# Kernel tuning notes

Hardware: AMD Instinct MI355X
Metric: run time of the kernel (lower is better)

## Reference

```python
import jax, jax.numpy as jnp
import numpy as np

B, N, L, G, H, D, DIM = 32, 512, 4096, 128, 8, 1, 64
ALPHA = 3.0


def setup_inputs() -> dict:
    key = jax.random.key(0)
    k = jax.random.split(key, 8)
    return {
        "idx": jnp.arange(N, dtype=jnp.int32),
        "queries": jnp.zeros((1,), jnp.float32),
        "keys": jnp.zeros((1,), jnp.float32),
        "values": jnp.zeros((1,), jnp.float32),
        "attn_mask": jnp.zeros((1,), jnp.bool_),
        "x": jax.random.normal(k[0], (B, N, L), jnp.float32),
        "emb1": jax.random.normal(k[1], (N, DIM), jnp.float32),
        "emb2": jax.random.normal(k[2], (N, DIM), jnp.float32),
        "lin1_w": jax.random.normal(k[3], (DIM, DIM), jnp.float32) / np.sqrt(DIM).astype(np.float32),
        "lin1_b": jnp.zeros((DIM,), jnp.float32),
        "lin2_w": jax.random.normal(k[4], (DIM, DIM), jnp.float32) / np.sqrt(DIM).astype(np.float32),
        "lin2_b": jnp.zeros((DIM,), jnp.float32),
        "mlp_w": jax.random.normal(k[5], (L, H * D), jnp.float32) / np.sqrt(L).astype(np.float32),
        "mlp_b": jnp.zeros((H * D,), jnp.float32),
        "W_sel": jax.random.normal(k[6], (H, G, D), jnp.float32),
    }


def reference(idx, queries, keys, values, attn_mask, x,
              emb1, emb2, lin1_w, lin1_b, lin2_w, lin2_b,
              mlp_w, mlp_b, W_sel):
    # --- graph_constructor.forward(idx) ---
    n1 = jnp.tanh(ALPHA * (emb1[idx] @ lin1_w + lin1_b))   # [N, DIM]
    n2 = jnp.tanh(ALPHA * (emb2[idx] @ lin2_w + lin2_b))   # [N, DIM]
    a = n1 @ n2.T - n2 @ n1.T                               # [N, N]
    adj = jnp.tanh(ALPHA * a)
    # topk (k == nsensor in GlobalAttention) + scatter mask; noise in the
    # original only perturbs tie-breaking of indices, values are set to 1.
    kk = idx.shape[0]
    _, top_idx = jax.lax.top_k(adj, kk)
    rows = jnp.arange(adj.shape[0])[:, None]
    mask = jnp.zeros_like(adj).at[rows, top_idx].set(1.0)
    adj = adj * mask

    # --- SelectAttention(x) ---
    b, n, l = x.shape
    newx = jnp.tanh(x.reshape(b * n, l) @ mlp_w + mlp_b)    # [(B N), H*D]
    # faithful raw row-major reshape (matches torch.reshape semantics)
    newx = newx.reshape(b, H, n, D)                          # [B, H, N, D]
    sel = jax.nn.relu(jnp.einsum('bhnd,hgd->bhng', newx, W_sel))[:, 0]  # [B, N, G]

    # --- combine ---
    scores = jnp.einsum('ls,blg->bsg', adj, sel)             # [B, N, G]
    series = jax.nn.softmax(scores, axis=-1)
    V = jnp.einsum('bls,blg->bsg', x, series)                # [B, L, G]
    return V
```

## Files before the change

### kernel.cpp

```cpp
#include <hip/hip_runtime.h>
#include <hip/hip_bf16.h>
#include <math.h>

#define BB 32
#define NN 512
#define LL 4096
#define GG 128
#define DD 64
#define AS 36
#define RS2 36

typedef __attribute__((ext_vector_type(4))) float f32x4;
typedef __attribute__((ext_vector_type(8))) short bf16x8;
typedef __attribute__((ext_vector_type(4))) unsigned u32x4;
typedef __attribute__((ext_vector_type(4))) unsigned short u16x4;

__device__ inline float sx(float v, int m) { return __shfl_xor(v, m, 64); }

__global__ __launch_bounds__(64) void ga_nodes(
    const int* __restrict__ idx,
    const float* __restrict__ emb1, const float* __restrict__ emb2,
    const float* __restrict__ w1, const float* __restrict__ b1,
    const float* __restrict__ w2, const float* __restrict__ b2,
    float* __restrict__ n1, float* __restrict__ n2,
    float* __restrict__ n1T, float* __restrict__ n2T) {
  int i = blockIdx.x;
  int d = threadIdx.x;
  int ii = idx[i];
  const float* e1 = emb1 + ii * DD;
  const float* e2 = emb2 + ii * DD;
  float a1 = 0.f, a2 = 0.f;
  #pragma unroll 8
  for (int k = 0; k < DD; ++k) {
    a1 += e1[k] * w1[k * DD + d];
    a2 += e2[k] * w2[k * DD + d];
  }
  float v1 = tanhf(3.f * (a1 + b1[d]));
  float v2 = tanhf(3.f * (a2 + b2[d]));
  n1[i * DD + d] = v1;
  n2[i * DD + d] = v2;
  n1T[(size_t)d * NN + i] = v1;
  n2T[(size_t)d * NN + i] = v2;
}

__global__ __launch_bounds__(256) void ga_adjT(
    const float* __restrict__ n1, const float* __restrict__ n2,
    const float* __restrict__ n1T, const float* __restrict__ n2T,
    __hip_bfloat16* __restrict__ adjT16) {
  int l0 = blockIdx.x * 64, s0 = blockIdx.y * 16;
  int tid = threadIdx.x;
  int ll = tid & 63;
  int sw = __builtin_amdgcn_readfirstlane(tid >> 6);
  int l = l0 + ll;

  float d1[4] = {0.f, 0.f, 0.f, 0.f}, d2[4] = {0.f, 0.f, 0.f, 0.f};
  #pragma unroll
  for (int kb = 0; kb < 4; ++kb) {
    float a1[16], a2[16];
    #pragma unroll
    for (int k = 0; k < 16; ++k) {
      a1[k] = n1T[(size_t)(kb * 16 + k) * NN + l];
      a2[k] = n2T[(size_t)(kb * 16 + k) * NN + l];
    }
    #pragma unroll
    for (int si = 0; si < 4; ++si) {
      int s = s0 + sw * 4 + si;
      const float* s1 = n1 + (size_t)s * DD + kb * 16;
      const float* s2 = n2 + (size_t)s * DD + kb * 16;
      #pragma unroll
      for (int k = 0; k < 16; ++k) {
        d1[si] += a1[k] * s2[k];
        d2[si] += a2[k] * s1[k];
      }
    }
  }
  #pragma unroll
  for (int si = 0; si < 4; ++si) {
    int s = s0 + sw * 4 + si;
    adjT16[(size_t)s * NN + l] =
        __float2bfloat16(tanhf(3.f * (d1[si] - d2[si])));
  }
}

__global__ __launch_bounds__(256) void ga_mlp(
    const float* __restrict__ x, const float* __restrict__ mlp_w,
    const float* __restrict__ mlp_b, const float* __restrict__ wsel,
    __hip_bfloat16* __restrict__ RT) {
  int b = blockIdx.y;
  int j0 = blockIdx.x * 4;
  int n0 = j0 * 8;
  int tid = threadIdx.x;
  const float* xb = x + (size_t)b * NN * LL;

  float acc[4][8];
  #pragma unroll
  for (int r = 0; r < 4; ++r)
    #pragma unroll
    for (int c = 0; c < 8; ++c) acc[r][c] = 0.f;

  #pragma unroll 4
  for (int it = 0; it < 16; ++it) {
    int l = it * 256 + tid;
    float4 w0 = *(const float4*)(mlp_w + (size_t)l * 8);
    float4 w1 = *(const float4*)(mlp_w + (size_t)l * 8 + 4);
    float wv[8] = {w0.x, w0.y, w0.z, w0.w, w1.x, w1.y, w1.z, w1.w};
    float xv[4];
    #pragma unroll
    for (int r = 0; r < 4; ++r) xv[r] = xb[(size_t)(j0 + r) * LL + l];
    #pragma unroll
    for (int r = 0; r < 4; ++r)
      #pragma unroll
      for (int c = 0; c < 8; ++c) acc[r][c] += xv[r] * wv[c];
  }
  #pragma unroll
  for (int r = 0; r < 4; ++r)
    #pragma unroll
    for (int c = 0; c < 8; ++c) {
      float v = acc[r][c];
      for (int off = 32; off; off >>= 1) v += __shfl_down(v, off);
      acc[r][c] = v;
    }
  __shared__ float red[4][32];
  __shared__ float tl[32];
  int lane = tid & 63, wave = tid >> 6;
  if (lane == 0) {
    #pragma unroll
    for (int r = 0; r < 4; ++r)
      #pragma unroll
      for (int c = 0; c < 8; ++c) red[wave][r * 8 + c] = acc[r][c];
  }
  __syncthreads();
  if (tid < 32) {
    float s = red[0][tid] + red[1][tid] + red[2][tid] + red[3][tid];
    tl[tid] = tanhf(s + mlp_b[tid & 7]);
  }
  __syncthreads();
  unsigned short* rp = (unsigned short*)RT + (size_t)b * GG * NN + n0;
  #pragma unroll
  for (int itw = 0; itw < 4; ++itw) {
    int f = itw * 256 + tid;
    int g = f >> 3, c4 = (f & 7) * 4;
    float w = wsel[g];
    u16x4 pk;
    #pragma unroll
    for (int k = 0; k < 4; ++k)
      pk[k] = __bfloat16_as_ushort(__float2bfloat16(fmaxf(tl[c4 + k] * w, 0.f)));
    *(u16x4*)(rp + (size_t)g * NN + c4) = pk;
  }
}

__global__ __launch_bounds__(256) void ga_scores_mfma(
    const __hip_bfloat16* __restrict__ adjT16,
    const __hip_bfloat16* __restrict__ RT,
    __hip_bfloat16* __restrict__ seriesT) {
  int b = blockIdx.y;
  int s0 = blockIdx.x * 64;
  int tid = threadIdx.x;
  __shared__ unsigned As[64 * AS];
  __shared__ unsigned Bs[128 * AS];
  int wave = tid >> 6, lane = tid & 63, q = lane >> 4, mrow = lane & 15;
  const unsigned short* ap = (const unsigned short*)adjT16;
  const unsigned short* bp = (const unsigned short*)RT + (size_t)b * GG * NN;

  f32x4 acc[8];
  #pragma unroll
  for (int nf = 0; nf < 8; ++nf) acc[nf] = (f32x4){0.f, 0.f, 0.f, 0.f};

  for (int l0 = 0; l0 < NN; l0 += 64) {
    #pragma unroll
    for (int it = 0; it < 2; ++it) {
      int ci = it * 256 + tid;
      int row = ci >> 3, part = ci & 7;
      *(u32x4*)&As[row * AS + part * 4] =
          *(const u32x4*)(ap + (size_t)(s0 + row) * NN + l0 + part * 8);
    }
    #pragma unroll
    for (int it = 0; it < 4; ++it) {
      int ci = it * 256 + tid;
      int row = ci >> 3, part = ci & 7;
      *(u32x4*)&Bs[row * AS + part * 4] =
          *(const u32x4*)(bp + (size_t)row * NN + l0 + part * 8);
    }
    __syncthreads();
    #pragma unroll
    for (int ks = 0; ks < 2; ++ks) {
      bf16x8 af = *(const bf16x8*)&As[(wave * 16 + mrow) * AS + ks * 16 + q * 4];
      #pragma unroll
      for (int nf = 0; nf < 8; ++nf) {
        bf16x8 bfr = *(const bf16x8*)&Bs[(nf * 16 + mrow) * AS + ks * 16 + q * 4];
        acc[nf] = __builtin_amdgcn_mfma_f32_16x16x32_bf16(af, bfr, acc[nf], 0, 0, 0);
      }
    }
    __syncthreads();
  }

  unsigned short* sT = (unsigned short*)seriesT + (size_t)b * GG * NN;
  f32x4 mx = acc[0];
  #pragma unroll
  for (int nf = 1; nf < 8; ++nf)
    #pragma unroll
    for (int r = 0; r < 4; ++r) mx[r] = fmaxf(mx[r], acc[nf][r]);
  #pragma unroll
  for (int m = 1; m <= 8; m <<= 1)
    #pragma unroll
    for (int r = 0; r < 4; ++r) mx[r] = fmaxf(mx[r], sx(mx[r], m));
  f32x4 sum = (f32x4){0.f, 0.f, 0.f, 0.f};
  #pragma unroll
  for (int nf = 0; nf < 8; ++nf)
    #pragma unroll
    for (int r = 0; r < 4; ++r) {
      float e = __expf(acc[nf][r] - mx[r]);
      acc[nf][r] = e;
      sum[r] += e;
    }
  #pragma unroll
  for (int m = 1; m <= 8; m <<= 1)
    #pragma unroll
    for (int r = 0; r < 4; ++r) sum[r] += sx(sum[r], m);
  f32x4 inv;
  #pragma unroll
  for (int r = 0; r < 4; ++r) inv[r] = 1.f / sum[r];
  int sbase = s0 + wave * 16 + q * 4;
  #pragma unroll
  for (int nf = 0; nf < 8; ++nf) {
    u16x4 pk;
    #pragma unroll
    for (int r = 0; r < 4; ++r)
      pk[r] = __bfloat16_as_ushort(__float2bfloat16(acc[nf][r] * inv[r]));
    *(u16x4*)(sT + (size_t)(nf * 16 + mrow) * NN + sbase) = pk;
  }
}

__global__ __launch_bounds__(256) void ga_V_mfma(
    const float* __restrict__ x, const __hip_bfloat16* __restrict__ seriesT,
    float* __restrict__ out) {
  int b = blockIdx.y;
  int p0 = blockIdx.x * 128;
  int tid = threadIdx.x;
  __shared__ unsigned St[128 * RS2];
  int wave = tid >> 6, lane = tid & 63, q = lane >> 4, mrow = lane & 15;
  int sgrow = tid >> 1;
  int sc0 = (tid & 1) * 4;
  const float* xb = x + (size_t)b * NN * LL;
  const unsigned short* sb = (const unsigned short*)seriesT + (size_t)b * GG * NN;
  int pcol = p0 + wave * 32 + mrow;

  f32x4 acc[2][8];
  #pragma unroll
  for (int mf = 0; mf < 2; ++mf)
    #pragma unroll
    for (int nf = 0; nf < 8; ++nf) acc[mf][nf] = (f32x4){0.f, 0.f, 0.f, 0.f};

  #pragma unroll 1
  for (int l0 = 0; l0 < NN; l0 += 64) {
    float xv[2][2][8];
    #pragma unroll
    for (int mf = 0; mf < 2; ++mf)
      #pragma unroll
      for (int ks = 0; ks < 2; ++ks) {
        const float* xp = xb + (size_t)(l0 + ks * 32 + q * 8) * LL + pcol + mf * 16;
        #pragma unroll
        for (int jj = 0; jj < 8; ++jj) xv[mf][ks][jj] = xp[(size_t)jj * LL];
      }
    u32x4 sv[4];
    #pragma unroll
    for (int k = 0; k < 4; ++k)
      sv[k] = *(const u32x4*)(sb + (size_t)sgrow * NN + l0 + (sc0 + k) * 8);
    #pragma unroll
    for (int k = 0; k < 4; ++k)
      *(u32x4*)&St[sgrow * RS2 + (sc0 + k) * 4] = sv[k];
    __syncthreads();

    bf16x8 af[2][2];
    #pragma unroll
    for (int mf = 0; mf < 2; ++mf)
      #pragma unroll
      for (int ks = 0; ks < 2; ++ks) {
        unsigned w[4];
        #pragma unroll
        for (int t = 0; t < 4; ++t) {
          __hip_bfloat162 pk = __float22bfloat162_rn(
              make_float2(xv[mf][ks][2 * t], xv[mf][ks][2 * t + 1]));
          w[t] = *(unsigned*)&pk;
        }
        af[mf][ks] = *(bf16x8*)w;
      }
    #pragma unroll
    for (int ks = 0; ks < 2; ++ks)
      #pragma unroll
      for (int nf = 0; nf < 8; ++nf) {
        bf16x8 bfr = *(const bf16x8*)&St[(nf * 16 + mrow) * RS2 + ks * 16 + q * 4];
        acc[0][nf] = __builtin_amdgcn_mfma_f32_16x16x32_bf16(af[0][ks], bfr, acc[0][nf], 0, 0, 0);
        acc[1][nf] = __builtin_amdgcn_mfma_f32_16x16x32_bf16(af[1][ks], bfr, acc[1][nf], 0, 0, 0);
      }
    __syncthreads();
  }

  #pragma unroll
  for (int mf = 0; mf < 2; ++mf) {
    int pb = p0 + wave * 32 + mf * 16 + q * 4;
    #pragma unroll
    for (int nf = 0; nf < 8; ++nf) {
      int g = nf * 16 + mrow;
      float* op = out + ((size_t)b * LL + pb) * GG + g;
      #pragma unroll
      for (int r = 0; r < 4; ++r) op[(size_t)r * GG] = acc[mf][nf][r];
    }
  }
}

extern "C" void kernel_launch(void* const* d_in, const int* in_sizes, int n_in,
                              void* d_out, int out_size, void* d_ws, size_t ws_size,
                              hipStream_t stream) {
  const int*   idx    = (const int*)d_in[0];
  const float* x      = (const float*)d_in[5];
  const float* emb1   = (const float*)d_in[6];
  const float* emb2   = (const float*)d_in[7];
  const float* lin1_w = (const float*)d_in[8];
  const float* lin1_b = (const float*)d_in[9];
  const float* lin2_w = (const float*)d_in[10];
  const float* lin2_b = (const float*)d_in[11];
  const float* mlp_w  = (const float*)d_in[12];
  const float* mlp_b  = (const float*)d_in[13];
  const float* W_sel  = (const float*)d_in[14];
  float* out = (float*)d_out;

  float* ws = (float*)d_ws;
  float* n1  = ws;
  float* n2  = ws + 32768;
  float* n1T = ws + 65536;
  float* n2T = ws + 98304;
  __hip_bfloat16* adjT16  = (__hip_bfloat16*)(ws + 131072);
  __hip_bfloat16* RT      = (__hip_bfloat16*)(ws + 262144);
  __hip_bfloat16* seriesT = (__hip_bfloat16*)(ws + 1310720);

  ga_nodes<<<NN, 64, 0, stream>>>(idx, emb1, emb2, lin1_w, lin1_b,
                                  lin2_w, lin2_b, n1, n2, n1T, n2T);
  ga_adjT<<<dim3(NN / 64, NN / 16), 256, 0, stream>>>(n1, n2, n1T, n2T, adjT16);
  ga_mlp<<<dim3(16, BB), 256, 0, stream>>>(x, mlp_w, mlp_b, W_sel, RT);
  ga_scores_mfma<<<dim3(8, BB), 256, 0, stream>>>(adjT16, RT, seriesT);
  ga_V_mfma<<<dim3(LL / 128, BB), 256, 0, stream>>>(x, seriesT, out);
}
```

Baseline: 114.7 us.

## Fuse node embedding into adjacency kernel and build sel operand on the fly

Merges the node-embedding kernel into the adjacency kernel. Each block recomputes the 80 node rows it needs into shared memory, which removes one launch and the n1/n2 transposed buffers. The MLP kernel now writes only the 32 tanh values per row, and the scores MFMA kernel builds the relu(t*W_sel) bf16 B-fragments in registers instead of reading a materialized RT tensor from global memory. This cuts global traffic and a launch, but adds redundant embedding compute across blocks and extra ALU work inside the MFMA loop.

```diff
diff --git a/kernel.cpp b/kernel.cpp
--- a/kernel.cpp
+++ b/kernel.cpp
@@ -17,75 +17,74 @@
 
 __device__ inline float sx(float v, int m) { return __shfl_xor(v, m, 64); }
 
-__global__ __launch_bounds__(64) void ga_nodes(
+__global__ __launch_bounds__(256) void ga_graph(
     const int* __restrict__ idx,
     const float* __restrict__ emb1, const float* __restrict__ emb2,
     const float* __restrict__ w1, const float* __restrict__ b1,
     const float* __restrict__ w2, const float* __restrict__ b2,
-    float* __restrict__ n1, float* __restrict__ n2,
-    float* __restrict__ n1T, float* __restrict__ n2T) {
-  int i = blockIdx.x;
-  int d = threadIdx.x;
-  int ii = idx[i];
-  const float* e1 = emb1 + ii * DD;
-  const float* e2 = emb2 + ii * DD;
-  float a1 = 0.f, a2 = 0.f;
-  #pragma unroll 8
-  for (int k = 0; k < DD; ++k) {
-    a1 += e1[k] * w1[k * DD + d];
-    a2 += e2[k] * w2[k * DD + d];
-  }
-  float v1 = tanhf(3.f * (a1 + b1[d]));
-  float v2 = tanhf(3.f * (a2 + b2[d]));
-  n1[i * DD + d] = v1;
-  n2[i * DD + d] = v2;
-  n1T[(size_t)d * NN + i] = v1;
-  n2T[(size_t)d * NN + i] = v2;
-}
-
-__global__ __launch_bounds__(256) void ga_adjT(
-    const float* __restrict__ n1, const float* __restrict__ n2,
-    const float* __restrict__ n1T, const float* __restrict__ n2T,
     __hip_bfloat16* __restrict__ adjT16) {
   int l0 = blockIdx.x * 64, s0 = blockIdx.y * 16;
   int tid = threadIdx.x;
-  int ll = tid & 63;
-  int sw = __builtin_amdgcn_readfirstlane(tid >> 6);
-  int l = l0 + ll;
-
+  int d = tid & 63;
+  int rw = tid >> 6;
+
+  __shared__ float n1L[64][65], n2L[64][65];
+  __shared__ float n1S[16][64], n2S[16][64];
+
+  #pragma unroll 1
+  for (int rr = 0; rr < 80; rr += 4) {
+    int r = rr + rw;
+    int gi = (r < 64) ? (l0 + r) : (s0 + r - 64);
+    int ii = idx[gi];
+    const float* e1 = emb1 + (size_t)ii * DD;
+    const float* e2 = emb2 + (size_t)ii * DD;
+    float a1 = 0.f, a2 = 0.f;
+    #pragma unroll 8
+    for (int k = 0; k < DD; ++k) {
+      a1 += e1[k] * w1[k * DD + d];
+      a2 += e2[k] * w2[k * DD + d];
+    }
+    float v1 = tanhf(3.f * (a1 + b1[d]));
+    float v2 = tanhf(3.f * (a2 + b2[d]));
+    if (r < 64) {
+      n1L[r][d] = v1; n2L[r][d] = v2;
+    } else {
+      n1S[r - 64][d] = v1; n2S[r - 64][d] = v2;
+    }
+  }
+  __syncthreads();
+
+  int ll = d;
   float d1[4] = {0.f, 0.f, 0.f, 0.f}, d2[4] = {0.f, 0.f, 0.f, 0.f};
   #pragma unroll
   for (int kb = 0; kb < 4; ++kb) {
     float a1[16], a2[16];
     #pragma unroll
     for (int k = 0; k < 16; ++k) {
-      a1[k] = n1T[(size_t)(kb * 16 + k) * NN + l];
-      a2[k] = n2T[(size_t)(kb * 16 + k) * NN + l];
+      a1[k] = n1L[ll][kb * 16 + k];
+      a2[k] = n2L[ll][kb * 16 + k];
     }
     #pragma unroll
     for (int si = 0; si < 4; ++si) {
-      int s = s0 + sw * 4 + si;
-      const float* s1 = n1 + (size_t)s * DD + kb * 16;
-      const float* s2 = n2 + (size_t)s * DD + kb * 16;
+      int sr = rw * 4 + si;
       #pragma unroll
       for (int k = 0; k < 16; ++k) {
-        d1[si] += a1[k] * s2[k];
-        d2[si] += a2[k] * s1[k];
+        d1[si] += a1[k] * n2S[sr][kb * 16 + k];
+        d2[si] += a2[k] * n1S[sr][kb * 16 + k];
       }
     }
   }
   #pragma unroll
   for (int si = 0; si < 4; ++si) {
-    int s = s0 + sw * 4 + si;
-    adjT16[(size_t)s * NN + l] =
+    int s = s0 + rw * 4 + si;
+    adjT16[(size_t)s * NN + l0 + ll] =
         __float2bfloat16(tanhf(3.f * (d1[si] - d2[si])));
   }
 }
 
 __global__ __launch_bounds__(256) void ga_mlp(
     const float* __restrict__ x, const float* __restrict__ mlp_w,
-    const float* __restrict__ mlp_b, const float* __restrict__ wsel,
-    __hip_bfloat16* __restrict__ RT) {
+    const float* __restrict__ mlp_b, float* __restrict__ t_out) {
   int b = blockIdx.y;
   int j0 = blockIdx.x * 4;
   int n0 = j0 * 8;
@@ -121,7 +120,6 @@
       acc[r][c] = v;
     }
   __shared__ float red[4][32];
-  __shared__ float tl[32];
   int lane = tid & 63, wave = tid >> 6;
   if (lane == 0) {
     #pragma unroll
@@ -132,35 +130,27 @@
   __syncthreads();
   if (tid < 32) {
     float s = red[0][tid] + red[1][tid] + red[2][tid] + red[3][tid];
-    tl[tid] = tanhf(s + mlp_b[tid & 7]);
-  }
-  __syncthreads();
-  unsigned short* rp = (unsigned short*)RT + (size_t)b * GG * NN + n0;
-  #pragma unroll
-  for (int itw = 0; itw < 4; ++itw) {
-    int f = itw * 256 + tid;
-    int g = f >> 3, c4 = (f & 7) * 4;
-    float w = wsel[g];
-    u16x4 pk;
-    #pragma unroll
-    for (int k = 0; k < 4; ++k)
-      pk[k] = __bfloat16_as_ushort(__float2bfloat16(fmaxf(tl[c4 + k] * w, 0.f)));
-    *(u16x4*)(rp + (size_t)g * NN + c4) = pk;
+    t_out[(size_t)b * NN + n0 + tid] = tanhf(s + mlp_b[tid & 7]);
   }
 }
 
 __global__ __launch_bounds__(256) void ga_scores_mfma(
     const __hip_bfloat16* __restrict__ adjT16,
-    const __hip_bfloat16* __restrict__ RT,
+    const float* __restrict__ t, const float* __restrict__ wsel,
     __hip_bfloat16* __restrict__ seriesT) {
   int b = blockIdx.y;
   int s0 = blockIdx.x * 64;
   int tid = threadIdx.x;
   __shared__ unsigned As[64 * AS];
-  __shared__ unsigned Bs[128 * AS];
+  __shared__ float tl[NN];
   int wave = tid >> 6, lane = tid & 63, q = lane >> 4, mrow = lane & 15;
   const unsigned short* ap = (const unsigned short*)adjT16;
-  const unsigned short* bp = (const unsigned short*)RT + (size_t)b * GG * NN;
+
+  tl[tid] = t[(size_t)b * NN + tid];
+  tl[256 + tid] = t[(size_t)b * NN + 256 + tid];
+  float wg[8];
+  #pragma unroll
+  for (int nf = 0; nf < 8; ++nf) wg[nf] = wsel[nf * 16 + mrow];
 
   f32x4 acc[8];
   #pragma unroll
@@ -174,20 +164,25 @@
       *(u32x4*)&As[row * AS + part * 4] =
           *(const u32x4*)(ap + (size_t)(s0 + row) * NN + l0 + part * 8);
     }
-    #pragma unroll
-    for (int it = 0; it < 4; ++it) {
-      int ci = it * 256 + tid;
-      int row = ci >> 3, part = ci & 7;
-      *(u32x4*)&Bs[row * AS + part * 4] =
-          *(const u32x4*)(bp + (size_t)row * NN + l0 + part * 8);
-    }
     __syncthreads();
     #pragma unroll
     for (int ks = 0; ks < 2; ++ks) {
       bf16x8 af = *(const bf16x8*)&As[(wave * 16 + mrow) * AS + ks * 16 + q * 4];
+      float tv[8];
+      int lb = l0 + ks * 32 + q * 8;
+      #pragma unroll
+      for (int j = 0; j < 8; ++j) tv[j] = tl[lb + j];
       #pragma unroll
       for (int nf = 0; nf < 8; ++nf) {
-        bf16x8 bfr = *(const bf16x8*)&Bs[(nf * 16 + mrow) * AS + ks * 16 + q * 4];
+        unsigned w[4];
+        #pragma unroll
+        for (int p2 = 0; p2 < 4; ++p2) {
+          __hip_bfloat162 pk = __float22bfloat162_rn(make_float2(
+              fmaxf(tv[2 * p2] * wg[nf], 0.f),
+              fmaxf(tv[2 * p2 + 1] * wg[nf], 0.f)));
+          w[p2] = *(unsigned*)&pk;
+        }
+        bf16x8 bfr = *(bf16x8*)w;
         acc[nf] = __builtin_amdgcn_mfma_f32_16x16x32_bf16(af, bfr, acc[nf], 0, 0, 0);
       }
     }
@@ -326,18 +321,13 @@
   float* out = (float*)d_out;
 
   float* ws = (float*)d_ws;
-  float* n1  = ws;
-  float* n2  = ws + 32768;
-  float* n1T = ws + 65536;
-  float* n2T = ws + 98304;
-  __hip_bfloat16* adjT16  = (__hip_bfloat16*)(ws + 131072);
-  __hip_bfloat16* RT      = (__hip_bfloat16*)(ws + 262144);
-  __hip_bfloat16* seriesT = (__hip_bfloat16*)(ws + 1310720);
-
-  ga_nodes<<<NN, 64, 0, stream>>>(idx, emb1, emb2, lin1_w, lin1_b,
-                                  lin2_w, lin2_b, n1, n2, n1T, n2T);
-  ga_adjT<<<dim3(NN / 64, NN / 16), 256, 0, stream>>>(n1, n2, n1T, n2T, adjT16);
-  ga_mlp<<<dim3(16, BB), 256, 0, stream>>>(x, mlp_w, mlp_b, W_sel, RT);
-  ga_scores_mfma<<<dim3(8, BB), 256, 0, stream>>>(adjT16, RT, seriesT);
+  float* t = ws;
+  __hip_bfloat16* adjT16  = (__hip_bfloat16*)(ws + 16384);
+  __hip_bfloat16* seriesT = (__hip_bfloat16*)(ws + 147456);
+
+  ga_graph<<<dim3(NN / 64, NN / 16), 256, 0, stream>>>(
+      idx, emb1, emb2, lin1_w, lin1_b, lin2_w, lin2_b, adjT16);
+  ga_mlp<<<dim3(16, BB), 256, 0, stream>>>(x, mlp_w, mlp_b, t);
+  ga_scores_mfma<<<dim3(8, BB), 256, 0, stream>>>(adjT16, t, W_sel, seriesT);
   ga_V_mfma<<<dim3(LL / 128, BB), 256, 0, stream>>>(x, seriesT, out);
 }
```

Result: slower. 161.7 us (+41.0%).

## Compute selection matrix on the fly in scores kernel instead of materializing RT

Applied to the files above, without the earlier changes.

The MLP kernel now writes only the tanh outputs t[B,N] instead of expanding them into a bf16 RT[B,G,N] tensor via W_sel. The scores kernel loads t into shared memory and builds the MFMA B fragments in registers as relu(t*w_g), so it no longer stages RT tiles through shared memory. This removes the write and re-read of an 4 MB intermediate and the B-tile shared-memory traffic. In exchange it adds per-MFMA conversion ALU work in the inner loop.

```diff
diff --git a/kernel.cpp b/kernel.cpp
--- a/kernel.cpp
+++ b/kernel.cpp
@@ -84,8 +84,7 @@
 
 __global__ __launch_bounds__(256) void ga_mlp(
     const float* __restrict__ x, const float* __restrict__ mlp_w,
-    const float* __restrict__ mlp_b, const float* __restrict__ wsel,
-    __hip_bfloat16* __restrict__ RT) {
+    const float* __restrict__ mlp_b, float* __restrict__ t_out) {
   int b = blockIdx.y;
   int j0 = blockIdx.x * 4;
   int n0 = j0 * 8;
@@ -121,7 +120,6 @@
       acc[r][c] = v;
     }
   __shared__ float red[4][32];
-  __shared__ float tl[32];
   int lane = tid & 63, wave = tid >> 6;
   if (lane == 0) {
     #pragma unroll
@@ -132,35 +130,27 @@
   __syncthreads();
   if (tid < 32) {
     float s = red[0][tid] + red[1][tid] + red[2][tid] + red[3][tid];
-    tl[tid] = tanhf(s + mlp_b[tid & 7]);
-  }
-  __syncthreads();
-  unsigned short* rp = (unsigned short*)RT + (size_t)b * GG * NN + n0;
-  #pragma unroll
-  for (int itw = 0; itw < 4; ++itw) {
-    int f = itw * 256 + tid;
-    int g = f >> 3, c4 = (f & 7) * 4;
-    float w = wsel[g];
-    u16x4 pk;
-    #pragma unroll
-    for (int k = 0; k < 4; ++k)
-      pk[k] = __bfloat16_as_ushort(__float2bfloat16(fmaxf(tl[c4 + k] * w, 0.f)));
-    *(u16x4*)(rp + (size_t)g * NN + c4) = pk;
+    t_out[(size_t)b * NN + n0 + tid] = tanhf(s + mlp_b[tid & 7]);
   }
 }
 
 __global__ __launch_bounds__(256) void ga_scores_mfma(
     const __hip_bfloat16* __restrict__ adjT16,
-    const __hip_bfloat16* __restrict__ RT,
+    const float* __restrict__ t, const float* __restrict__ wsel,
     __hip_bfloat16* __restrict__ seriesT) {
   int b = blockIdx.y;
   int s0 = blockIdx.x * 64;
   int tid = threadIdx.x;
   __shared__ unsigned As[64 * AS];
-  __shared__ unsigned Bs[128 * AS];
+  __shared__ float tl[NN];
   int wave = tid >> 6, lane = tid & 63, q = lane >> 4, mrow = lane & 15;
   const unsigned short* ap = (const unsigned short*)adjT16;
-  const unsigned short* bp = (const unsigned short*)RT + (size_t)b * GG * NN;
+
+  tl[tid] = t[(size_t)b * NN + tid];
+  tl[256 + tid] = t[(size_t)b * NN + 256 + tid];
+  float wg[8];
+  #pragma unroll
+  for (int nf = 0; nf < 8; ++nf) wg[nf] = wsel[nf * 16 + mrow];
 
   f32x4 acc[8];
   #pragma unroll
@@ -174,20 +164,25 @@
       *(u32x4*)&As[row * AS + part * 4] =
           *(const u32x4*)(ap + (size_t)(s0 + row) * NN + l0 + part * 8);
     }
-    #pragma unroll
-    for (int it = 0; it < 4; ++it) {
-      int ci = it * 256 + tid;
-      int row = ci >> 3, part = ci & 7;
-      *(u32x4*)&Bs[row * AS + part * 4] =
-          *(const u32x4*)(bp + (size_t)row * NN + l0 + part * 8);
-    }
     __syncthreads();
     #pragma unroll
     for (int ks = 0; ks < 2; ++ks) {
       bf16x8 af = *(const bf16x8*)&As[(wave * 16 + mrow) * AS + ks * 16 + q * 4];
+      float tv[8];
+      int lb = l0 + ks * 32 + q * 8;
+      #pragma unroll
+      for (int j = 0; j < 8; ++j) tv[j] = tl[lb + j];
       #pragma unroll
       for (int nf = 0; nf < 8; ++nf) {
-        bf16x8 bfr = *(const bf16x8*)&Bs[(nf * 16 + mrow) * AS + ks * 16 + q * 4];
+        unsigned w[4];
+        #pragma unroll
+        for (int p2 = 0; p2 < 4; ++p2) {
+          __hip_bfloat162 pk = __float22bfloat162_rn(make_float2(
+              fmaxf(tv[2 * p2] * wg[nf], 0.f),
+              fmaxf(tv[2 * p2 + 1] * wg[nf], 0.f)));
+          w[p2] = *(unsigned*)&pk;
+        }
+        bf16x8 bfr = *(bf16x8*)w;
         acc[nf] = __builtin_amdgcn_mfma_f32_16x16x32_bf16(af, bfr, acc[nf], 0, 0, 0);
       }
     }
@@ -330,14 +325,14 @@
   float* n2  = ws + 32768;
   float* n1T = ws + 65536;
   float* n2T = ws + 98304;
-  __hip_bfloat16* adjT16  = (__hip_bfloat16*)(ws + 131072);
-  __hip_bfloat16* RT      = (__hip_bfloat16*)(ws + 262144);
-  __hip_bfloat16* seriesT = (__hip_bfloat16*)(ws + 1310720);
+  float* t   = ws + 131072;
+  __hip_bfloat16* adjT16  = (__hip_bfloat16*)(ws + 147456);
+  __hip_bfloat16* seriesT = (__hip_bfloat16*)(ws + 212992);
 
   ga_nodes<<<NN, 64, 0, stream>>>(idx, emb1, emb2, lin1_w, lin1_b,
                                   lin2_w, lin2_b, n1, n2, n1T, n2T);
   ga_adjT<<<dim3(NN / 64, NN / 16), 256, 0, stream>>>(n1, n2, n1T, n2T, adjT16);
-  ga_mlp<<<dim3(16, BB), 256, 0, stream>>>(x, mlp_w, mlp_b, W_sel, RT);
-  ga_scores_mfma<<<dim3(8, BB), 256, 0, stream>>>(adjT16, RT, seriesT);
+  ga_mlp<<<dim3(16, BB), 256, 0, stream>>>(x, mlp_w, mlp_b, t);
+  ga_scores_mfma<<<dim3(8, BB), 256, 0, stream>>>(adjT16, t, W_sel, seriesT);
   ga_V_mfma<<<dim3(LL / 128, BB), 256, 0, stream>>>(x, seriesT, out);
 }
```

Result: slower. 119.6 us (+4.3%).
